# Kernel tuning notes

Hardware: AMD Instinct MI355X
Metric: run time of the kernel (lower is better)

## Reference

```python
import jax, jax.numpy as jnp
import numpy as np

BN_EPS = 1e-5


def setup_inputs() -> dict:
    key = jax.random.key(0)
    ks = jax.random.split(key, 14)
    B, N, C, NS = 2, 1024, 512, 64
    seed_xyz = jax.random.uniform(ks[0], (B, N, 3), jnp.float32)          # points in unit cube
    seed_features = jax.random.normal(ks[1], (B, C, N), jnp.float32)
    # per-seed rotation matrices (orthonormalized via QR)
    rot = jnp.linalg.qr(jax.random.normal(ks[2], (B, N, 3, 3), jnp.float32))[0]
    # cuboid extents sized so each query finds a reasonable neighbor count
    crop_size = 0.2 + 0.3 * jax.random.uniform(ks[3], (B, N, 3), jnp.float32)
    W1 = jax.random.normal(ks[4], (256, 3 + C), jnp.float32) / np.float32(np.sqrt(3 + C))
    gamma1 = 1.0 + 0.1 * jax.random.normal(ks[5], (256,), jnp.float32)
    beta1 = 0.1 * jax.random.normal(ks[6], (256,), jnp.float32)
    mean1 = 0.1 * jax.random.normal(ks[7], (256,), jnp.float32)
    var1 = 0.5 + jax.random.uniform(ks[8], (256,), jnp.float32)
    W2 = jax.random.normal(ks[9], (256, 256), jnp.float32) / np.float32(16.0)
    gamma2 = 1.0 + 0.1 * jax.random.normal(ks[10], (256,), jnp.float32)
    beta2 = 0.1 * jax.random.normal(ks[11], (256,), jnp.float32)
    mean2 = 0.1 * jax.random.normal(ks[12], (256,), jnp.float32)
    var2 = 0.5 + jax.random.uniform(ks[13], (256,), jnp.float32)
    return dict(seed_xyz=seed_xyz, seed_features=seed_features, rot=rot,
                crop_size=crop_size, W1=W1, gamma1=gamma1, beta1=beta1,
                mean1=mean1, var1=var1, W2=W2, gamma2=gamma2, beta2=beta2,
                mean2=mean2, var2=var2, nsample=NS)


def _conv_bn_relu(x, W, g, b, m, v):
    # 1x1 conv (no bias, bn=True) + inference BatchNorm + ReLU
    y = jnp.einsum('bpnc,oc->bpno', x, W)
    scale = g * jax.lax.rsqrt(v + BN_EPS)
    return jax.nn.relu((y - m) * scale + b)


def reference(seed_xyz, seed_features, rot, crop_size,
              W1, gamma1, beta1, mean1, var1,
              W2, gamma2, beta2, mean2, var2, nsample):
    # ---- rotated rectangular query + group (queries == points == seed_xyz) ----
    # diff[b,p,n] = xyz[b,n] - query[b,p]; rotate into the query's local frame
    diff = seed_xyz[:, None, :, :] - seed_xyz[:, :, None, :]          # (B,P,N,3)
    local = jnp.einsum('bpnj,bpjk->bpnk', diff, rot)                  # (B,P,N,3)
    inside = jnp.all(jnp.abs(local) <= 0.5 * crop_size[:, :, None, :], axis=-1)  # (B,P,N)
    # first `nsample` in-region indices, invalid slots filled with the first hit
    order = jnp.argsort(jnp.where(inside, 0, 1).astype(jnp.int32), axis=-1, stable=True)
    idx = order[..., :nsample]                                        # (B,P,NS)
    valid = jnp.take_along_axis(inside, idx, axis=-1)
    idx = jnp.where(valid, idx, idx[..., :1])
    # gather rotated local xyz and features
    g_xyz = jnp.take_along_axis(local, idx[..., None], axis=2)        # (B,P,NS,3)
    feats = jnp.swapaxes(seed_features, 1, 2)                         # (B,N,C)
    g_feat = jax.vmap(lambda f, i: f[i])(feats, idx)                  # (B,P,NS,C)
    grouped = jnp.concatenate([g_xyz, g_feat], axis=-1)               # (B,P,NS,3+C)
    # ---- SharedMLP (1x1 conv + BN + ReLU) x2, then max over samples ----
    h = _conv_bn_relu(grouped, W1, gamma1, beta1, mean1, var1)
    h = _conv_bn_relu(h, W2, gamma2, beta2, mean2, var2)
    out = jnp.max(h, axis=2)                                          # (B,P,256)
    return jnp.swapaxes(out, 1, 2)                                    # (B,256,P)
```

## Files before the change

### kernel.cpp

```cpp
#include <hip/hip_runtime.h>
#include <hip/hip_bf16.h>
#include <math.h>

typedef __attribute__((ext_vector_type(8))) __bf16 bf16x8;
typedef __attribute__((ext_vector_type(4))) __bf16 bf16x4;
typedef __attribute__((ext_vector_type(2))) __bf16 bf16x2;
typedef __attribute__((ext_vector_type(4))) float f32x4;

#define NPTS 1024
#define CIN 512
#define NSAMP 64
#define LDFT 520
#define LDFO 136

__device__ __forceinline__ void local_coords(const float* q, float cx, float cy, float cz,
                                             const float R[9], float& l0, float& l1, float& l2) {
    float d0 = __fsub_rn(q[0], cx);
    float d1 = __fsub_rn(q[1], cy);
    float d2 = __fsub_rn(q[2], cz);
    l0 = __fadd_rn(__fadd_rn(__fmul_rn(d0, R[0]), __fmul_rn(d1, R[3])), __fmul_rn(d2, R[6]));
    l1 = __fadd_rn(__fadd_rn(__fmul_rn(d0, R[1]), __fmul_rn(d1, R[4])), __fmul_rn(d2, R[7]));
    l2 = __fadd_rn(__fadd_rn(__fmul_rn(d0, R[2]), __fmul_rn(d1, R[5])), __fmul_rn(d2, R[8]));
}

__global__ __launch_bounds__(256) void setup_kernel(
    const float* __restrict__ xyz, const float* __restrict__ rot,
    const float* __restrict__ crop,
    const float* __restrict__ W1, const float* __restrict__ W2,
    const float* __restrict__ g1, const float* __restrict__ be1,
    const float* __restrict__ m1, const float* __restrict__ v1,
    const float* __restrict__ g2, const float* __restrict__ be2,
    const float* __restrict__ m2, const float* __restrict__ v2,
    __bf16* __restrict__ W1f, __bf16* __restrict__ W2s,
    float* __restrict__ wxs,
    float* __restrict__ s1, float* __restrict__ b1,
    float* __restrict__ s2, float* __restrict__ b2,
    unsigned short* __restrict__ seln_g) {
    __shared__ unsigned long long msk[16];
    __shared__ int wpre[17];
    __shared__ int selr[NSAMP];

    const int t = threadIdx.x;
    if (blockIdx.x < 256) {
        const int o = blockIdx.x;
        if (t == 0) {
            float sc1 = g1[o] / sqrtf(v1[o] + 1e-5f);
            s1[o] = sc1;
            b1[o] = be1[o] - m1[o] * sc1;
            float sc2 = g2[o] / sqrtf(v2[o] + 1e-5f);
            s2[o] = sc2;
            b2[o] = be2[o] - m2[o] * sc2;
            wxs[o * 4 + 0] = sc1 * W1[o * 515 + 0];
            wxs[o * 4 + 1] = sc1 * W1[o * 515 + 1];
            wxs[o * 4 + 2] = sc1 * W1[o * 515 + 2];
            wxs[o * 4 + 3] = 0.f;
        }
        for (int k = t; k < CIN; k += blockDim.x)
            W1f[o * CIN + k] = (__bf16)W1[o * 515 + 3 + k];
        {
            const int f = o * 256 + t;
            const int j = f & 7;
            const int l = (f >> 3) & 63;
            const int nt = (f >> 9) & 1;
            const int ks = (f >> 10) & 7;
            const int w = (f >> 13) & 7;
            const int o2 = w * 32 + nt * 16 + (l & 15);
            const int k = ks * 32 + ((l >> 4) << 3) + j;
            W2s[f] = (__bf16)W2[o2 * 256 + k];
        }
        return;
    }
    const int bid = blockIdx.x - 256;
    const int b = bid >> 10;
    const int l = t & 63, w = t >> 6;

    const float cx = xyz[bid * 3 + 0], cy = xyz[bid * 3 + 1], cz = xyz[bid * 3 + 2];
    float R[9];
#pragma unroll
    for (int j = 0; j < 9; ++j) R[j] = rot[bid * 9 + j];
    const float h0 = 0.5f * crop[bid * 3 + 0];
    const float h1 = 0.5f * crop[bid * 3 + 1];
    const float h2 = 0.5f * crop[bid * 3 + 2];

#pragma unroll
    for (int i = 0; i < 4; ++i) {
        const int n = i * 256 + t;
        float l0, l1, l2;
        local_coords(xyz + (size_t)(b * NPTS + n) * 3, cx, cy, cz, R, l0, l1, l2);
        bool ins = (__builtin_fabsf(l0) <= h0) && (__builtin_fabsf(l1) <= h1) &&
                   (__builtin_fabsf(l2) <= h2);
        unsigned long long bal = __ballot(ins);
        if (l == 0) msk[i * 4 + w] = bal;
    }
    __syncthreads();
    if (t < 64) {
        const int c = (t < 16) ? __popcll(msk[t]) : 0;
        int sum = c;
#pragma unroll
        for (int d = 1; d < 16; d <<= 1) {
            int v = __shfl_up(sum, d);
            if (t >= d) sum += v;
        }
        if (t < 16) wpre[t] = sum - c;
        if (t == 15) wpre[16] = sum;
    }
    __syncthreads();
    const int cnt = wpre[16];
#pragma unroll
    for (int i = 0; i < 4; ++i) {
        const int n = i * 256 + t;
        const unsigned long long wd = msk[n >> 6];
        const int bit = n & 63;
        if ((wd >> bit) & 1ull) {
            int rank = wpre[n >> 6] + __popcll(wd & ((1ull << bit) - 1ull));
            if (rank < NSAMP) selr[rank] = n;
        }
    }
    __syncthreads();
    if (t < NSAMP) {
        const int n = (t < cnt) ? selr[t] : selr[0];
        seln_g[(size_t)bid * NSAMP + t] = (unsigned short)n;
    }
}

__global__ __launch_bounds__(256) void fgemm_kernel(const float* __restrict__ feats,
                                                    const __bf16* __restrict__ W1f,
                                                    const float* __restrict__ s1,
                                                    const float* __restrict__ b1,
                                                    __bf16* __restrict__ Fsb) {
    __shared__ __align__(16) __bf16 Ft[16][LDFT];
    __shared__ __align__(16) __bf16 Fo[16][LDFO];
    const int t = threadIdx.x;
    const int b = blockIdx.x >> 7;
    const int half = (blockIdx.x >> 6) & 1;
    const int n0 = (blockIdx.x & 63) << 4;
    const int l = t & 63, w = t >> 6;
    const int lo = l & 15, kg = l >> 4;

    const float* fb = feats + (size_t)b * (CIN * NPTS) + n0;

    {
        const int n = t & 15;
        const int cq = (t >> 4) * 2;
        for (int i = 0; i < 16; ++i) {
            int c = i * 32 + cq;
            float v0 = fb[(size_t)c * NPTS + n];
            float v1 = fb[(size_t)(c + 1) * NPTS + n];
            bf16x2 pk = {(__bf16)v0, (__bf16)v1};
            *(bf16x2*)(&Ft[n][c]) = pk;
        }
    }
    __syncthreads();

    f32x4 acc[2];
#pragma unroll
    for (int mt = 0; mt < 2; ++mt) acc[mt] = f32x4{0.f, 0.f, 0.f, 0.f};

#pragma unroll
    for (int ks = 0; ks < 16; ++ks) {
        const int kk = ks * 32 + kg * 8;
        const bf16x8 bfr = *(const bf16x8*)(&Ft[lo][kk]);
#pragma unroll
        for (int mt = 0; mt < 2; ++mt) {
            const int o = half * 128 + w * 32 + mt * 16 + lo;
            const bf16x8 af = *(const bf16x8*)(&W1f[(size_t)o * CIN + kk]);
            acc[mt] = __builtin_amdgcn_mfma_f32_16x16x32_bf16(af, bfr, acc[mt], 0, 0, 0);
        }
    }
    __syncthreads();
#pragma unroll
    for (int mt = 0; mt < 2; ++mt) {
        const int ol = w * 32 + mt * 16 + kg * 4;
        const f32x4 sv = *(const f32x4*)(&s1[half * 128 + ol]);
        const f32x4 bv = *(const f32x4*)(&b1[half * 128 + ol]);
        bf16x4 r;
#pragma unroll
        for (int j = 0; j < 4; ++j) r[j] = (__bf16)fmaf(acc[mt][j], sv[j], bv[j]);
        *(bf16x4*)(&Fo[lo][ol]) = r;
    }
    __syncthreads();
    {
        const int row = t >> 4, c = t & 15;
        const bf16x8 v = *(const bf16x8*)(&Fo[row][c * 8]);
        *(bf16x8*)(&Fsb[((size_t)(b * NPTS + n0 + row)) * 256 + half * 128 + c * 8]) = v;
    }
}

__global__ __launch_bounds__(512, 2) void fused_kernel(
    const float* __restrict__ xyz, const float* __restrict__ rot,
    const __bf16* __restrict__ Fsb, const float* __restrict__ wxs,
    const unsigned short* __restrict__ seln_g,
    const __bf16* __restrict__ W2s, const float* __restrict__ s2g, const float* __restrict__ b2g,
    float* __restrict__ out) {
    __shared__ __align__(16) char A2raw[NSAMP * 512];
    __shared__ __align__(16) f32x4 lcb[NSAMP];
    __shared__ __align__(16) float outst[256][4];

    const int raw = (int)blockIdx.x;
    const int pg = (raw & 7) * 64 + (raw >> 3);
    const int b = pg >> 8;
    const int p0 = (pg & 255) * 4;
    const int t = threadIdx.x;
    const int l = t & 63, w = t >> 6;
    const int lo = l & 15, kg = l >> 4;

    bf16x8 wf[8][2];
#pragma unroll
    for (int ks = 0; ks < 8; ++ks)
#pragma unroll
        for (int nt = 0; nt < 2; ++nt)
            wf[ks][nt] = *(const bf16x8*)(&W2s[(size_t)((((w * 8 + ks) * 2 + nt) * 64) + l) * 8]);

    const int oc = (t & 31) * 8;
    const int sg = t >> 5;
    f32x4 wv[8];
#pragma unroll
    for (int j = 0; j < 8; ++j) wv[j] = *(const f32x4*)(&wxs[(oc + j) * 4]);

    float sc[2], bb[2];
#pragma unroll
    for (int nt = 0; nt < 2; ++nt) {
        const int o = w * 32 + nt * 16 + lo;
        sc[nt] = s2g[o];
        bb[nt] = b2g[o];
    }

    bf16x8 stg[4];

    {
        const int p = p0;
        if (t < NSAMP) {
            const int n = (int)seln_g[((size_t)(b * NPTS + p)) * 64 + t];
            const int bid = b * NPTS + p;
            const float cx = xyz[bid * 3 + 0], cy = xyz[bid * 3 + 1], cz = xyz[bid * 3 + 2];
            float R[9];
#pragma unroll
            for (int j = 0; j < 9; ++j) R[j] = rot[bid * 9 + j];
            float l0, l1, l2;
            local_coords(xyz + (size_t)(b * NPTS + n) * 3, cx, cy, cz, R, l0, l1, l2);
            lcb[t] = f32x4{l0, l1, l2, 0.f};
        }
#pragma unroll
        for (int si = 0; si < 4; ++si) {
            const int s = sg * 4 + si;
            const int n = (int)seln_g[((size_t)(b * NPTS + p)) * 64 + s];
            stg[si] = *(const bf16x8*)(&Fsb[((size_t)(b * NPTS + n)) * 256 + oc]);
        }
        __syncthreads();
#pragma unroll
        for (int si = 0; si < 4; ++si) {
            const int s = sg * 4 + si;
            const f32x4 cd = lcb[s];
            bf16x8 pk;
#pragma unroll
            for (int j = 0; j < 8; ++j) {
                const float x = fmaf(cd.x, wv[j].x,
                                     fmaf(cd.y, wv[j].y, fmaf(cd.z, wv[j].z, (float)stg[si][j])));
                pk[j] = (__bf16)fmaxf(x, 0.f);
            }
            *(bf16x8*)(A2raw + s * 512 + ((oc * 2) ^ ((s & 7) << 4))) = pk;
        }
        __syncthreads();
    }

    for (int pi = 0; pi < 4; ++pi) {
        if (pi < 3) {
            const int p = p0 + pi + 1;
            if (t < NSAMP) {
                const int n = (int)seln_g[((size_t)(b * NPTS + p)) * 64 + t];
                const int bid = b * NPTS + p;
                const float cx = xyz[bid * 3 + 0], cy = xyz[bid * 3 + 1], cz = xyz[bid * 3 + 2];
                float R[9];
#pragma unroll
                for (int j = 0; j < 9; ++j) R[j] = rot[bid * 9 + j];
                float l0, l1, l2;
                local_coords(xyz + (size_t)(b * NPTS + n) * 3, cx, cy, cz, R, l0, l1, l2);
                lcb[t] = f32x4{l0, l1, l2, 0.f};
            }
#pragma unroll
            for (int si = 0; si < 4; ++si) {
                const int s = sg * 4 + si;
                const int n = (int)seln_g[((size_t)(b * NPTS + p)) * 64 + s];
                stg[si] = *(const bf16x8*)(&Fsb[((size_t)(b * NPTS + n)) * 256 + oc]);
            }
        }

        f32x4 acc[4][2];
#pragma unroll
        for (int mt = 0; mt < 4; ++mt)
#pragma unroll
            for (int nt = 0; nt < 2; ++nt)
                acc[mt][nt] = f32x4{0.f, 0.f, 0.f, 0.f};

#pragma unroll
        for (int ks = 0; ks < 8; ++ks) {
            const int kkb = ks * 64 + kg * 16;
            bf16x8 af[4];
#pragma unroll
            for (int mt = 0; mt < 4; ++mt) {
                const int row = mt * 16 + lo;
                af[mt] = *(const bf16x8*)(A2raw + row * 512 + (kkb ^ ((row & 7) << 4)));
            }
#pragma unroll
            for (int nt = 0; nt < 2; ++nt)
#pragma unroll
                for (int mt = 0; mt < 4; ++mt)
                    acc[mt][nt] = __builtin_amdgcn_mfma_f32_16x16x32_bf16(af[mt], wf[ks][nt],
                                                                          acc[mt][nt], 0, 0, 0);
        }

#pragma unroll
        for (int nt = 0; nt < 2; ++nt) {
            float mx = 0.f;
#pragma unroll
            for (int mt = 0; mt < 4; ++mt)
#pragma unroll
                for (int r = 0; r < 4; ++r)
                    mx = fmaxf(mx, fmaxf(fmaf(acc[mt][nt][r], sc[nt], bb[nt]), 0.f));
            mx = fmaxf(mx, __shfl_xor(mx, 16));
            mx = fmaxf(mx, __shfl_xor(mx, 32));
            if (kg == 0) outst[w * 32 + nt * 16 + lo][pi] = mx;
        }
        __syncthreads();

        if (pi < 3) {
#pragma unroll
            for (int si = 0; si < 4; ++si) {
                const int s = sg * 4 + si;
                const f32x4 cd = lcb[s];
                bf16x8 pk;
#pragma unroll
                for (int j = 0; j < 8; ++j) {
                    const float x = fmaf(cd.x, wv[j].x,
                                         fmaf(cd.y, wv[j].y, fmaf(cd.z, wv[j].z, (float)stg[si][j])));
                    pk[j] = (__bf16)fmaxf(x, 0.f);
                }
                *(bf16x8*)(A2raw + s * 512 + ((oc * 2) ^ ((s & 7) << 4))) = pk;
            }
        }
        __syncthreads();
    }

    if (t < 256) {
        const int o = t;
        const f32x4 v = *(const f32x4*)(&outst[o][0]);
        *(f32x4*)(&out[((size_t)b * 256 + o) * NPTS + p0]) = v;
    }
}

extern "C" void kernel_launch(void* const* d_in, const int* in_sizes, int n_in,
                              void* d_out, int out_size, void* d_ws, size_t ws_size,
                              hipStream_t stream) {
    (void)in_sizes; (void)n_in; (void)out_size; (void)ws_size;
    const float* xyz   = (const float*)d_in[0];
    const float* feats = (const float*)d_in[1];
    const float* rot   = (const float*)d_in[2];
    const float* crop  = (const float*)d_in[3];
    const float* W1    = (const float*)d_in[4];
    const float* g1    = (const float*)d_in[5];
    const float* be1   = (const float*)d_in[6];
    const float* m1    = (const float*)d_in[7];
    const float* v1    = (const float*)d_in[8];
    const float* W2    = (const float*)d_in[9];
    const float* g2    = (const float*)d_in[10];
    const float* be2   = (const float*)d_in[11];
    const float* m2    = (const float*)d_in[12];
    const float* v2    = (const float*)d_in[13];

    char* ws = (char*)d_ws;
    __bf16* W1f = (__bf16*)(ws + 0);
    __bf16* W2s = (__bf16*)(ws + 262144);
    float*  wxs = (float*)(ws + 393216);
    float*  s1  = (float*)(ws + 397312);
    float*  b1  = (float*)(ws + 398336);
    float*  s2  = (float*)(ws + 399360);
    float*  b2  = (float*)(ws + 400384);
    __bf16* Fsb = (__bf16*)(ws + 401408);
    unsigned short* seln = (unsigned short*)(ws + 1449984);

    setup_kernel<<<2304, 256, 0, stream>>>(xyz, rot, crop,
                                           W1, W2, g1, be1, m1, v1, g2, be2, m2, v2,
                                           W1f, W2s, wxs, s1, b1, s2, b2, seln);
    fgemm_kernel<<<256, 256, 0, stream>>>(feats, W1f, s1, b1, Fsb);
    fused_kernel<<<512, 512, 0, stream>>>(xyz, rot, Fsb, wxs, seln, W2s, s2, b2,
                                          (float*)d_out);
}
```

Baseline: 44.05 us.

## Fuse ball-query selection into main kernel and skip empty sample tiles

Removes the separate setup kernel. The rectangular query, prefix scan and neighbor selection now run inside the fused kernel, which handles 8 query points per block instead of 4. The fused kernel also computes BN scales and converts W2 to bf16 directly from the raw inputs, and a tiny kernel converts only W1. MFMA tiles beyond the actual in-region count are skipped, which avoids redundant rows that would only duplicate the first hit. The trade-off is more per-block prologue work, redundant weight conversion in every block, and half as many blocks.

Result: slower. 51.52 us (+17.0%).

```diff
diff --git a/kernel.cpp b/kernel.cpp
--- a/kernel.cpp
+++ b/kernel.cpp
@@ -23,113 +23,27 @@
     l2 = __fadd_rn(__fadd_rn(__fmul_rn(d0, R[2]), __fmul_rn(d1, R[5])), __fmul_rn(d2, R[8]));
 }
 
-__global__ __launch_bounds__(256) void setup_kernel(
-    const float* __restrict__ xyz, const float* __restrict__ rot,
-    const float* __restrict__ crop,
-    const float* __restrict__ W1, const float* __restrict__ W2,
-    const float* __restrict__ g1, const float* __restrict__ be1,
-    const float* __restrict__ m1, const float* __restrict__ v1,
-    const float* __restrict__ g2, const float* __restrict__ be2,
-    const float* __restrict__ m2, const float* __restrict__ v2,
-    __bf16* __restrict__ W1f, __bf16* __restrict__ W2s,
-    float* __restrict__ wxs,
-    float* __restrict__ s1, float* __restrict__ b1,
-    float* __restrict__ s2, float* __restrict__ b2,
-    unsigned short* __restrict__ seln_g) {
-    __shared__ unsigned long long msk[16];
-    __shared__ int wpre[17];
-    __shared__ int selr[NSAMP];
-
-    const int t = threadIdx.x;
-    if (blockIdx.x < 256) {
-        const int o = blockIdx.x;
-        if (t == 0) {
-            float sc1 = g1[o] / sqrtf(v1[o] + 1e-5f);
-            s1[o] = sc1;
-            b1[o] = be1[o] - m1[o] * sc1;
-            float sc2 = g2[o] / sqrtf(v2[o] + 1e-5f);
-            s2[o] = sc2;
-            b2[o] = be2[o] - m2[o] * sc2;
-            wxs[o * 4 + 0] = sc1 * W1[o * 515 + 0];
-            wxs[o * 4 + 1] = sc1 * W1[o * 515 + 1];
-            wxs[o * 4 + 2] = sc1 * W1[o * 515 + 2];
-            wxs[o * 4 + 3] = 0.f;
-        }
-        for (int k = t; k < CIN; k += blockDim.x)
-            W1f[o * CIN + k] = (__bf16)W1[o * 515 + 3 + k];
-        {
-            const int f = o * 256 + t;
-            const int j = f & 7;
-            const int l = (f >> 3) & 63;
-            const int nt = (f >> 9) & 1;
-            const int ks = (f >> 10) & 7;
-            const int w = (f >> 13) & 7;
-            const int o2 = w * 32 + nt * 16 + (l & 15);
-            const int k = ks * 32 + ((l >> 4) << 3) + j;
-            W2s[f] = (__bf16)W2[o2 * 256 + k];
-        }
-        return;
-    }
-    const int bid = blockIdx.x - 256;
-    const int b = bid >> 10;
-    const int l = t & 63, w = t >> 6;
-
-    const float cx = xyz[bid * 3 + 0], cy = xyz[bid * 3 + 1], cz = xyz[bid * 3 + 2];
-    float R[9];
-#pragma unroll
-    for (int j = 0; j < 9; ++j) R[j] = rot[bid * 9 + j];
-    const float h0 = 0.5f * crop[bid * 3 + 0];
-    const float h1 = 0.5f * crop[bid * 3 + 1];
-    const float h2 = 0.5f * crop[bid * 3 + 2];
-
-#pragma unroll
-    for (int i = 0; i < 4; ++i) {
-        const int n = i * 256 + t;
-        float l0, l1, l2;
-        local_coords(xyz + (size_t)(b * NPTS + n) * 3, cx, cy, cz, R, l0, l1, l2);
-        bool ins = (__builtin_fabsf(l0) <= h0) && (__builtin_fabsf(l1) <= h1) &&
-                   (__builtin_fabsf(l2) <= h2);
-        unsigned long long bal = __ballot(ins);
-        if (l == 0) msk[i * 4 + w] = bal;
-    }
-    __syncthreads();
-    if (t < 64) {
-        const int c = (t < 16) ? __popcll(msk[t]) : 0;
-        int sum = c;
-#pragma unroll
-        for (int d = 1; d < 16; d <<= 1) {
-            int v = __shfl_up(sum, d);
-            if (t >= d) sum += v;
-        }
-        if (t < 16) wpre[t] = sum - c;
-        if (t == 15) wpre[16] = sum;
-    }
-    __syncthreads();
-    const int cnt = wpre[16];
-#pragma unroll
-    for (int i = 0; i < 4; ++i) {
-        const int n = i * 256 + t;
-        const unsigned long long wd = msk[n >> 6];
-        const int bit = n & 63;
-        if ((wd >> bit) & 1ull) {
-            int rank = wpre[n >> 6] + __popcll(wd & ((1ull << bit) - 1ull));
-            if (rank < NSAMP) selr[rank] = n;
-        }
-    }
-    __syncthreads();
-    if (t < NSAMP) {
-        const int n = (t < cnt) ? selr[t] : selr[0];
-        seln_g[(size_t)bid * NSAMP + t] = (unsigned short)n;
-    }
+__global__ __launch_bounds__(256) void w1cvt_kernel(const float* __restrict__ W1,
+                                                    __bf16* __restrict__ W1f) {
+    const int i4 = ((int)blockIdx.x * 256 + (int)threadIdx.x) * 4;
+    const int row = i4 >> 9, c = i4 & 511;
+    const float* src = W1 + (size_t)row * 515 + 3 + c;
+    bf16x4 v;
+#pragma unroll
+    for (int j = 0; j < 4; ++j) v[j] = (__bf16)src[j];
+    *(bf16x4*)(&W1f[i4]) = v;
 }
 
 __global__ __launch_bounds__(256) void fgemm_kernel(const float* __restrict__ feats,
                                                     const __bf16* __restrict__ W1f,
-                                                    const float* __restrict__ s1,
-                                                    const float* __restrict__ b1,
+                                                    const float* __restrict__ g1,
+                                                    const float* __restrict__ be1,
+                                                    const float* __restrict__ m1,
+                                                    const float* __restrict__ v1,
                                                     __bf16* __restrict__ Fsb) {
     __shared__ __align__(16) __bf16 Ft[16][LDFT];
     __shared__ __align__(16) __bf16 Fo[16][LDFO];
+    __shared__ float s1l[128], b1l[128];
     const int t = threadIdx.x;
     const int b = blockIdx.x >> 7;
     const int half = (blockIdx.x >> 6) & 1;
@@ -137,16 +51,22 @@
     const int l = t & 63, w = t >> 6;
     const int lo = l & 15, kg = l >> 4;
 
+    if (t < 128) {
+        const int o = half * 128 + t;
+        const float s = g1[o] / sqrtf(v1[o] + 1e-5f);
+        s1l[t] = s;
+        b1l[t] = be1[o] - m1[o] * s;
+    }
+
     const float* fb = feats + (size_t)b * (CIN * NPTS) + n0;
-
     {
         const int n = t & 15;
         const int cq = (t >> 4) * 2;
         for (int i = 0; i < 16; ++i) {
             int c = i * 32 + cq;
             float v0 = fb[(size_t)c * NPTS + n];
-            float v1 = fb[(size_t)(c + 1) * NPTS + n];
-            bf16x2 pk = {(__bf16)v0, (__bf16)v1};
+            float v1v = fb[(size_t)(c + 1) * NPTS + n];
+            bf16x2 pk = {(__bf16)v0, (__bf16)v1v};
             *(bf16x2*)(&Ft[n][c]) = pk;
         }
     }
@@ -171,8 +91,8 @@
 #pragma unroll
     for (int mt = 0; mt < 2; ++mt) {
         const int ol = w * 32 + mt * 16 + kg * 4;
-        const f32x4 sv = *(const f32x4*)(&s1[half * 128 + ol]);
-        const f32x4 bv = *(const f32x4*)(&b1[half * 128 + ol]);
+        const f32x4 sv = *(const f32x4*)(&s1l[ol]);
+        const f32x4 bv = *(const f32x4*)(&b1l[ol]);
         bf16x4 r;
 #pragma unroll
         for (int j = 0; j < 4; ++j) r[j] = (__bf16)fmaf(acc[mt][j], sv[j], bv[j]);
@@ -188,18 +108,25 @@
 
 __global__ __launch_bounds__(512, 2) void fused_kernel(
     const float* __restrict__ xyz, const float* __restrict__ rot,
-    const __bf16* __restrict__ Fsb, const float* __restrict__ wxs,
-    const unsigned short* __restrict__ seln_g,
-    const __bf16* __restrict__ W2s, const float* __restrict__ s2g, const float* __restrict__ b2g,
+    const float* __restrict__ crop,
+    const float* __restrict__ W1, const float* __restrict__ W2,
+    const float* __restrict__ g1, const float* __restrict__ v1,
+    const float* __restrict__ g2, const float* __restrict__ be2,
+    const float* __restrict__ m2, const float* __restrict__ v2,
+    const __bf16* __restrict__ Fsb,
     float* __restrict__ out) {
     __shared__ __align__(16) char A2raw[NSAMP * 512];
-    __shared__ __align__(16) f32x4 lcb[NSAMP];
-    __shared__ __align__(16) float outst[256][4];
+    __shared__ __align__(16) f32x4 lcsel[8][NSAMP];
+    __shared__ __align__(16) float outst[256][8];
+    __shared__ unsigned long long msk8[8][16];
+    __shared__ int wpre8[8][17];
+    __shared__ int sel8[8][NSAMP];
+    __shared__ int cnt8[8];
 
     const int raw = (int)blockIdx.x;
-    const int pg = (raw & 7) * 64 + (raw >> 3);
-    const int b = pg >> 8;
-    const int p0 = (pg & 255) * 4;
+    const int pg = (raw & 7) * 32 + (raw >> 3);
+    const int b = pg >> 7;
+    const int p0 = (pg & 127) * 8;
     const int t = threadIdx.x;
     const int l = t & 63, w = t >> 6;
     const int lo = l & 15, kg = l >> 4;
@@ -208,80 +135,145 @@
 #pragma unroll
     for (int ks = 0; ks < 8; ++ks)
 #pragma unroll
-        for (int nt = 0; nt < 2; ++nt)
-            wf[ks][nt] = *(const bf16x8*)(&W2s[(size_t)((((w * 8 + ks) * 2 + nt) * 64) + l) * 8]);
+        for (int nt = 0; nt < 2; ++nt) {
+            const int o2 = w * 32 + nt * 16 + lo;
+            const int k = ks * 32 + kg * 8;
+            const f32x4 a = *(const f32x4*)(&W2[(size_t)o2 * 256 + k]);
+            const f32x4 c = *(const f32x4*)(&W2[(size_t)o2 * 256 + k + 4]);
+            bf16x8 v;
+#pragma unroll
+            for (int j = 0; j < 4; ++j) { v[j] = (__bf16)a[j]; v[4 + j] = (__bf16)c[j]; }
+            wf[ks][nt] = v;
+        }
 
     const int oc = (t & 31) * 8;
     const int sg = t >> 5;
     f32x4 wv[8];
 #pragma unroll
-    for (int j = 0; j < 8; ++j) wv[j] = *(const f32x4*)(&wxs[(oc + j) * 4]);
+    for (int j = 0; j < 8; ++j) {
+        const int o = oc + j;
+        const float s1 = g1[o] / sqrtf(v1[o] + 1e-5f);
+        wv[j] = f32x4{s1 * W1[(size_t)o * 515 + 0], s1 * W1[(size_t)o * 515 + 1],
+                      s1 * W1[(size_t)o * 515 + 2], 0.f};
+    }
 
     float sc[2], bb[2];
 #pragma unroll
     for (int nt = 0; nt < 2; ++nt) {
         const int o = w * 32 + nt * 16 + lo;
-        sc[nt] = s2g[o];
-        bb[nt] = b2g[o];
-    }
-
-    bf16x8 stg[4];
-
-    {
-        const int p = p0;
-        if (t < NSAMP) {
-            const int n = (int)seln_g[((size_t)(b * NPTS + p)) * 64 + t];
-            const int bid = b * NPTS + p;
-            const float cx = xyz[bid * 3 + 0], cy = xyz[bid * 3 + 1], cz = xyz[bid * 3 + 2];
-            float R[9];
-#pragma unroll
-            for (int j = 0; j < 9; ++j) R[j] = rot[bid * 9 + j];
+        const float s2 = g2[o] / sqrtf(v2[o] + 1e-5f);
+        sc[nt] = s2;
+        bb[nt] = be2[o] - m2[o] * s2;
+    }
+
+    unsigned ins_bits = 0;
+#pragma unroll
+    for (int pi = 0; pi < 8; ++pi) {
+        const int bidp = b * NPTS + p0 + pi;
+        const float cx = xyz[bidp * 3 + 0], cy = xyz[bidp * 3 + 1], cz = xyz[bidp * 3 + 2];
+        float R[9];
+#pragma unroll
+        for (int j = 0; j < 9; ++j) R[j] = rot[bidp * 9 + j];
+        const float h0 = 0.5f * crop[bidp * 3 + 0];
+        const float h1 = 0.5f * crop[bidp * 3 + 1];
+        const float h2 = 0.5f * crop[bidp * 3 + 2];
+#pragma unroll
+        for (int i = 0; i < 2; ++i) {
+            const int n = i * 512 + t;
             float l0, l1, l2;
             local_coords(xyz + (size_t)(b * NPTS + n) * 3, cx, cy, cz, R, l0, l1, l2);
-            lcb[t] = f32x4{l0, l1, l2, 0.f};
-        }
+            bool ins = (__builtin_fabsf(l0) <= h0) && (__builtin_fabsf(l1) <= h1) &&
+                       (__builtin_fabsf(l2) <= h2);
+            unsigned long long bal = __ballot(ins);
+            if (l == 0) msk8[pi][i * 8 + w] = bal;
+            ins_bits |= ((unsigned)ins) << (pi * 2 + i);
+        }
+    }
+    __syncthreads();
+    {
+        const int pi = w;
+        int c = (l < 16) ? __popcll(msk8[pi][l]) : 0;
+        int sum = c;
+#pragma unroll
+        for (int d = 1; d < 16; d <<= 1) {
+            int v = __shfl_up(sum, d);
+            if (l >= d) sum += v;
+        }
+        if (l < 16) wpre8[pi][l] = sum - c;
+        if (l == 15) cnt8[pi] = sum;
+    }
+    __syncthreads();
+#pragma unroll
+    for (int pi = 0; pi < 8; ++pi) {
+#pragma unroll
+        for (int i = 0; i < 2; ++i) {
+            if ((ins_bits >> (pi * 2 + i)) & 1u) {
+                const int n = i * 512 + t;
+                const unsigned long long wd = msk8[pi][n >> 6];
+                const int rank = wpre8[pi][n >> 6] +
+                                 __popcll(wd & ((1ull << (n & 63)) - 1ull));
+                if (rank < NSAMP) {
+                    const int bidp = b * NPTS + p0 + pi;
+                    const float cx = xyz[bidp * 3 + 0], cy = xyz[bidp * 3 + 1],
+                                cz = xyz[bidp * 3 + 2];
+                    float R[9];
+#pragma unroll
+                    for (int j = 0; j < 9; ++j) R[j] = rot[bidp * 9 + j];
+                    float l0, l1, l2;
+                    local_coords(xyz + (size_t)(b * NPTS + n) * 3, cx, cy, cz, R, l0, l1, l2);
+                    sel8[pi][rank] = n;
+                    lcsel[pi][rank] = f32x4{l0, l1, l2, 0.f};
+                }
+            }
+        }
+    }
+    __syncthreads();
+
+    bf16x8 stg[4];
+    {
+        const int rn = min(cnt8[0], NSAMP);
+        const int rpad = (rn + 15) & ~15;
 #pragma unroll
         for (int si = 0; si < 4; ++si) {
             const int s = sg * 4 + si;
-            const int n = (int)seln_g[((size_t)(b * NPTS + p)) * 64 + s];
-            stg[si] = *(const bf16x8*)(&Fsb[((size_t)(b * NPTS + n)) * 256 + oc]);
-        }
-        __syncthreads();
+            if (s < rpad) {
+                const int n = (s < rn) ? sel8[0][s] : sel8[0][0];
+                stg[si] = *(const bf16x8*)(&Fsb[((size_t)(b * NPTS + n)) * 256 + oc]);
+            }
+        }
 #pragma unroll
         for (int si = 0; si < 4; ++si) {
             const int s = sg * 4 + si;
-            const f32x4 cd = lcb[s];
-            bf16x8 pk;
-#pragma unroll
-            for (int j = 0; j < 8; ++j) {
-                const float x = fmaf(cd.x, wv[j].x,
-                                     fmaf(cd.y, wv[j].y, fmaf(cd.z, wv[j].z, (float)stg[si][j])));
-                pk[j] = (__bf16)fmaxf(x, 0.f);
-            }
-            *(bf16x8*)(A2raw + s * 512 + ((oc * 2) ^ ((s & 7) << 4))) = pk;
-        }
-        __syncthreads();
-    }
-
-    for (int pi = 0; pi < 4; ++pi) {
-        if (pi < 3) {
-            const int p = p0 + pi + 1;
-            if (t < NSAMP) {
-                const int n = (int)seln_g[((size_t)(b * NPTS + p)) * 64 + t];
-                const int bid = b * NPTS + p;
-                const float cx = xyz[bid * 3 + 0], cy = xyz[bid * 3 + 1], cz = xyz[bid * 3 + 2];
-                float R[9];
-#pragma unroll
-                for (int j = 0; j < 9; ++j) R[j] = rot[bid * 9 + j];
-                float l0, l1, l2;
-                local_coords(xyz + (size_t)(b * NPTS + n) * 3, cx, cy, cz, R, l0, l1, l2);
-                lcb[t] = f32x4{l0, l1, l2, 0.f};
-            }
+            if (s < rpad) {
+                const f32x4 cd = (s < rn) ? lcsel[0][s] : lcsel[0][0];
+                bf16x8 pk;
+#pragma unroll
+                for (int j = 0; j < 8; ++j) {
+                    const float x = fmaf(cd.x, wv[j].x,
+                                         fmaf(cd.y, wv[j].y,
+                                              fmaf(cd.z, wv[j].z, (float)stg[si][j])));
+                    pk[j] = (__bf16)fmaxf(x, 0.f);
+                }
+                *(bf16x8*)(A2raw + s * 512 + ((oc * 2) ^ ((s & 7) << 4))) = pk;
+            }
+        }
+    }
+    __syncthreads();
+
+    for (int pi = 0; pi < 8; ++pi) {
+        const int mtmax = (min(cnt8[pi], NSAMP) + 15) >> 4;
+
+        int rpadn = 0, rn_next = 0;
+        if (pi < 7) {
+            rn_next = min(cnt8[pi + 1], NSAMP);
+            rpadn = (rn_next + 15) & ~15;
 #pragma unroll
             for (int si = 0; si < 4; ++si) {
                 const int s = sg * 4 + si;
-                const int n = (int)seln_g[((size_t)(b * NPTS + p)) * 64 + s];
-                stg[si] = *(const bf16x8*)(&Fsb[((size_t)(b * NPTS + n)) * 256 + oc]);
+                if (s < rpadn) {
+                    const int n = (s < rn_next) ? sel8[pi + 1][s] : sel8[pi + 1][0];
+                    stg[si] = *(const bf16x8*)(&Fsb[((size_t)(b * NPTS + n)) * 256 + oc]);
+                }
             }
         }
 
@@ -293,58 +285,63 @@
                 acc[mt][nt] = f32x4{0.f, 0.f, 0.f, 0.f};
 
 #pragma unroll
-        for (int ks = 0; ks < 8; ++ks) {
-            const int kkb = ks * 64 + kg * 16;
-            bf16x8 af[4];
-#pragma unroll
-            for (int mt = 0; mt < 4; ++mt) {
+        for (int mt = 0; mt < 4; ++mt) {
+            if (mt < mtmax) {
                 const int row = mt * 16 + lo;
-                af[mt] = *(const bf16x8*)(A2raw + row * 512 + (kkb ^ ((row & 7) << 4)));
-            }
-#pragma unroll
-            for (int nt = 0; nt < 2; ++nt)
-#pragma unroll
-                for (int mt = 0; mt < 4; ++mt)
-                    acc[mt][nt] = __builtin_amdgcn_mfma_f32_16x16x32_bf16(af[mt], wf[ks][nt],
-                                                                          acc[mt][nt], 0, 0, 0);
+#pragma unroll
+                for (int ks = 0; ks < 8; ++ks) {
+                    const bf16x8 a = *(const bf16x8*)(A2raw + row * 512 +
+                                                      ((ks * 64 + kg * 16) ^ ((row & 7) << 4)));
+                    acc[mt][0] = __builtin_amdgcn_mfma_f32_16x16x32_bf16(a, wf[ks][0],
+                                                                         acc[mt][0], 0, 0, 0);
+                    acc[mt][1] = __builtin_amdgcn_mfma_f32_16x16x32_bf16(a, wf[ks][1],
+                                                                         acc[mt][1], 0, 0, 0);
+                }
+            }
         }
 
 #pragma unroll
         for (int nt = 0; nt < 2; ++nt) {
             float mx = 0.f;
 #pragma unroll
-            for (int mt = 0; mt < 4; ++mt)
-#pragma unroll
-                for (int r = 0; r < 4; ++r)
-                    mx = fmaxf(mx, fmaxf(fmaf(acc[mt][nt][r], sc[nt], bb[nt]), 0.f));
+            for (int mt = 0; mt < 4; ++mt) {
+                if (mt < mtmax) {
+#pragma unroll
+                    for (int r = 0; r < 4; ++r)
+                        mx = fmaxf(mx, fmaxf(fmaf(acc[mt][nt][r], sc[nt], bb[nt]), 0.f));
+                }
+            }
             mx = fmaxf(mx, __shfl_xor(mx, 16));
             mx = fmaxf(mx, __shfl_xor(mx, 32));
             if (kg == 0) outst[w * 32 + nt * 16 + lo][pi] = mx;
         }
         __syncthreads();
 
-        if (pi < 3) {
+        if (pi < 7) {
 #pragma unroll
             for (int si = 0; si < 4; ++si) {
                 const int s = sg * 4 + si;
-                const f32x4 cd = lcb[s];
-                bf16x8 pk;
-#pragma unroll
-                for (int j = 0; j < 8; ++j) {
-                    const float x = fmaf(cd.x, wv[j].x,
-                                         fmaf(cd.y, wv[j].y, fmaf(cd.z, wv[j].z, (float)stg[si][j])));
-                    pk[j] = (__bf16)fmaxf(x, 0.f);
-                }
-                *(bf16x8*)(A2raw + s * 512 + ((oc * 2) ^ ((s & 7) << 4))) = pk;
+                if (s < rpadn) {
+                    const f32x4 cd = (s < rn_next) ? lcsel[pi + 1][s] : lcsel[pi + 1][0];
+                    bf16x8 pk;
+#pragma unroll
+                    for (int j = 0; j < 8; ++j) {
+                        const float x = fmaf(cd.x, wv[j].x,
+                                             fmaf(cd.y, wv[j].y,
+                                                  fmaf(cd.z, wv[j].z, (float)stg[si][j])));
+                        pk[j] = (__bf16)fmaxf(x, 0.f);
+                    }
+                    *(bf16x8*)(A2raw + s * 512 + ((oc * 2) ^ ((s & 7) << 4))) = pk;
+                }
             }
         }
         __syncthreads();
     }
 
-    if (t < 256) {
-        const int o = t;
-        const f32x4 v = *(const f32x4*)(&outst[o][0]);
-        *(f32x4*)(&out[((size_t)b * 256 + o) * NPTS + p0]) = v;
+    {
+        const int o = t >> 1, hf = t & 1;
+        const f32x4 v = *(const f32x4*)(&outst[o][hf * 4]);
+        *(f32x4*)(&out[((size_t)b * 256 + o) * NPTS + p0 + hf * 4]) = v;
     }
 }
 
@@ -369,19 +366,10 @@
 
     char* ws = (char*)d_ws;
     __bf16* W1f = (__bf16*)(ws + 0);
-    __bf16* W2s = (__bf16*)(ws + 262144);
-    float*  wxs = (float*)(ws + 393216);
-    float*  s1  = (float*)(ws + 397312);
-    float*  b1  = (float*)(ws + 398336);
-    float*  s2  = (float*)(ws + 399360);
-    float*  b2  = (float*)(ws + 400384);
-    __bf16* Fsb = (__bf16*)(ws + 401408);
-    unsigned short* seln = (unsigned short*)(ws + 1449984);
-
-    setup_kernel<<<2304, 256, 0, stream>>>(xyz, rot, crop,
-                                           W1, W2, g1, be1, m1, v1, g2, be2, m2, v2,
-                                           W1f, W2s, wxs, s1, b1, s2, b2, seln);
-    fgemm_kernel<<<256, 256, 0, stream>>>(feats, W1f, s1, b1, Fsb);
-    fused_kernel<<<512, 512, 0, stream>>>(xyz, rot, Fsb, wxs, seln, W2s, s2, b2,
-                                          (float*)d_out);
-}
+    __bf16* Fsb = (__bf16*)(ws + 262144);
+
+    w1cvt_kernel<<<128, 256, 0, stream>>>(W1, W1f);
+    fgemm_kernel<<<256, 256, 0, stream>>>(feats, W1f, g1, be1, m1, v1, Fsb);
+    fused_kernel<<<256, 512, 0, stream>>>(xyz, rot, crop, W1, W2, g1, v1, g2, be2, m2, v2,
+                                          Fsb, (float*)d_out);
+}
```

## Skip padded duplicate samples in fused MLP and precompute local coords in setup

Applied to the files above, without the earlier changes.

The setup kernel now stores each query's neighbor count and the rotated local coordinates of its selected neighbors, so the fused kernel no longer recomputes rotations from xyz/rot. The fused kernel preloads the selection indices, coordinates and counts for its four queries into shared memory. It then skips gathers, layer-1 epilogue work and second-layer MFMA tiles for rows beyond the valid count rounded up to 16. This relies on padded slots duplicating the first hit, which cannot change the max. It adds a global write and read of the coordinate buffer and branches whose benefit depends on how many neighbors each query has.

New measurement: 46.53 us. +5.6%, slower.

```diff
diff --git a/kernel.cpp b/kernel.cpp
--- a/kernel.cpp
+++ b/kernel.cpp
@@ -35,7 +35,9 @@
     float* __restrict__ wxs,
     float* __restrict__ s1, float* __restrict__ b1,
     float* __restrict__ s2, float* __restrict__ b2,
-    unsigned short* __restrict__ seln_g) {
+    unsigned short* __restrict__ seln_g, int* __restrict__ cnt_g,
+    f32x4* __restrict__ lcsel_g) {
+    __shared__ __align__(16) f32x4 lcall[NPTS];
     __shared__ unsigned long long msk[16];
     __shared__ int wpre[17];
     __shared__ int selr[NSAMP];
@@ -87,6 +89,7 @@
         const int n = i * 256 + t;
         float l0, l1, l2;
         local_coords(xyz + (size_t)(b * NPTS + n) * 3, cx, cy, cz, R, l0, l1, l2);
+        lcall[n] = f32x4{l0, l1, l2, 0.f};
         bool ins = (__builtin_fabsf(l0) <= h0) && (__builtin_fabsf(l1) <= h1) &&
                    (__builtin_fabsf(l2) <= h2);
         unsigned long long bal = __ballot(ins);
@@ -118,9 +121,11 @@
     }
     __syncthreads();
     if (t < NSAMP) {
-        const int n = (t < cnt) ? selr[t] : selr[0];
+        const int n = selr[(t < cnt) ? t : 0];
         seln_g[(size_t)bid * NSAMP + t] = (unsigned short)n;
-    }
+        lcsel_g[(size_t)bid * NSAMP + t] = lcall[n];
+    }
+    if (t == 0) cnt_g[bid] = cnt;
 }
 
 __global__ __launch_bounds__(256) void fgemm_kernel(const float* __restrict__ feats,
@@ -138,15 +143,14 @@
     const int lo = l & 15, kg = l >> 4;
 
     const float* fb = feats + (size_t)b * (CIN * NPTS) + n0;
-
     {
         const int n = t & 15;
         const int cq = (t >> 4) * 2;
         for (int i = 0; i < 16; ++i) {
             int c = i * 32 + cq;
             float v0 = fb[(size_t)c * NPTS + n];
-            float v1 = fb[(size_t)(c + 1) * NPTS + n];
-            bf16x2 pk = {(__bf16)v0, (__bf16)v1};
+            float v1v = fb[(size_t)(c + 1) * NPTS + n];
+            bf16x2 pk = {(__bf16)v0, (__bf16)v1v};
             *(bf16x2*)(&Ft[n][c]) = pk;
         }
     }
@@ -187,14 +191,16 @@
 }
 
 __global__ __launch_bounds__(512, 2) void fused_kernel(
-    const float* __restrict__ xyz, const float* __restrict__ rot,
     const __bf16* __restrict__ Fsb, const float* __restrict__ wxs,
-    const unsigned short* __restrict__ seln_g,
+    const unsigned short* __restrict__ seln_g, const int* __restrict__ cnt_g,
+    const f32x4* __restrict__ lcsel_g,
     const __bf16* __restrict__ W2s, const float* __restrict__ s2g, const float* __restrict__ b2g,
     float* __restrict__ out) {
     __shared__ __align__(16) char A2raw[NSAMP * 512];
-    __shared__ __align__(16) f32x4 lcb[NSAMP];
+    __shared__ __align__(16) f32x4 lcL[4][NSAMP];
     __shared__ __align__(16) float outst[256][4];
+    __shared__ unsigned short selL[4][NSAMP];
+    __shared__ int cntL[4];
 
     const int raw = (int)blockIdx.x;
     const int pg = (raw & 7) * 64 + (raw >> 3);
@@ -204,6 +210,14 @@
     const int l = t & 63, w = t >> 6;
     const int lo = l & 15, kg = l >> 4;
 
+    if (t < 256) {
+        const int pi = t >> 6, s = t & 63;
+        const size_t base = ((size_t)(b * NPTS + p0 + pi)) * NSAMP + s;
+        selL[pi][s] = seln_g[base];
+        lcL[pi][s] = lcsel_g[base];
+    }
+    if (t >= 256 && t < 260) cntL[t - 256] = cnt_g[b * NPTS + p0 + (t - 256)];
+
     bf16x8 wf[8][2];
 #pragma unroll
     for (int ks = 0; ks < 8; ++ks)
@@ -224,64 +238,51 @@
         sc[nt] = s2g[o];
         bb[nt] = b2g[o];
     }
+    __syncthreads();
 
     bf16x8 stg[4];
-
     {
-        const int p = p0;
-        if (t < NSAMP) {
-            const int n = (int)seln_g[((size_t)(b * NPTS + p)) * 64 + t];
-            const int bid = b * NPTS + p;
-            const float cx = xyz[bid * 3 + 0], cy = xyz[bid * 3 + 1], cz = xyz[bid * 3 + 2];
-            float R[9];
-#pragma unroll
-            for (int j = 0; j < 9; ++j) R[j] = rot[bid * 9 + j];
-            float l0, l1, l2;
-            local_coords(xyz + (size_t)(b * NPTS + n) * 3, cx, cy, cz, R, l0, l1, l2);
-            lcb[t] = f32x4{l0, l1, l2, 0.f};
-        }
+        const int rpad = (min(cntL[0], NSAMP) + 15) & ~15;
 #pragma unroll
         for (int si = 0; si < 4; ++si) {
             const int s = sg * 4 + si;
-            const int n = (int)seln_g[((size_t)(b * NPTS + p)) * 64 + s];
-            stg[si] = *(const bf16x8*)(&Fsb[((size_t)(b * NPTS + n)) * 256 + oc]);
-        }
-        __syncthreads();
+            if (s < rpad) {
+                const int n = (int)selL[0][s];
+                stg[si] = *(const bf16x8*)(&Fsb[((size_t)(b * NPTS + n)) * 256 + oc]);
+            }
+        }
 #pragma unroll
         for (int si = 0; si < 4; ++si) {
             const int s = sg * 4 + si;
-            const f32x4 cd = lcb[s];
-            bf16x8 pk;
-#pragma unroll
-            for (int j = 0; j < 8; ++j) {
-                const float x = fmaf(cd.x, wv[j].x,
-                                     fmaf(cd.y, wv[j].y, fmaf(cd.z, wv[j].z, (float)stg[si][j])));
-                pk[j] = (__bf16)fmaxf(x, 0.f);
-            }
-            *(bf16x8*)(A2raw + s * 512 + ((oc * 2) ^ ((s & 7) << 4))) = pk;
-        }
-        __syncthreads();
-    }
+            if (s < rpad) {
+                const f32x4 cd = lcL[0][s];
+                bf16x8 pk;
+#pragma unroll
+                for (int j = 0; j < 8; ++j) {
+                    const float x = fmaf(cd.x, wv[j].x,
+                                         fmaf(cd.y, wv[j].y,
+                                              fmaf(cd.z, wv[j].z, (float)stg[si][j])));
+                    pk[j] = (__bf16)fmaxf(x, 0.f);
+                }
+                *(bf16x8*)(A2raw + s * 512 + ((oc * 2) ^ ((s & 7) << 4))) = pk;
+            }
+        }
+    }
+    __syncthreads();
 
     for (int pi = 0; pi < 4; ++pi) {
+        const int mtmax = (min(cntL[pi], NSAMP) + 15) >> 4;
+
+        int rpadn = 0;
         if (pi < 3) {
-            const int p = p0 + pi + 1;
-            if (t < NSAMP) {
-                const int n = (int)seln_g[((size_t)(b * NPTS + p)) * 64 + t];
-                const int bid = b * NPTS + p;
-                const float cx = xyz[bid * 3 + 0], cy = xyz[bid * 3 + 1], cz = xyz[bid * 3 + 2];
-                float R[9];
-#pragma unroll
-                for (int j = 0; j < 9; ++j) R[j] = rot[bid * 9 + j];
-                float l0, l1, l2;
-                local_coords(xyz + (size_t)(b * NPTS + n) * 3, cx, cy, cz, R, l0, l1, l2);
-                lcb[t] = f32x4{l0, l1, l2, 0.f};
-            }
+            rpadn = (min(cntL[pi + 1], NSAMP) + 15) & ~15;
 #pragma unroll
             for (int si = 0; si < 4; ++si) {
                 const int s = sg * 4 + si;
-                const int n = (int)seln_g[((size_t)(b * NPTS + p)) * 64 + s];
-                stg[si] = *(const bf16x8*)(&Fsb[((size_t)(b * NPTS + n)) * 256 + oc]);
+                if (s < rpadn) {
+                    const int n = (int)selL[pi + 1][s];
+                    stg[si] = *(const bf16x8*)(&Fsb[((size_t)(b * NPTS + n)) * 256 + oc]);
+                }
             }
         }
 
@@ -293,30 +294,32 @@
                 acc[mt][nt] = f32x4{0.f, 0.f, 0.f, 0.f};
 
 #pragma unroll
-        for (int ks = 0; ks < 8; ++ks) {
-            const int kkb = ks * 64 + kg * 16;
-            bf16x8 af[4];
-#pragma unroll
-            for (int mt = 0; mt < 4; ++mt) {
+        for (int mt = 0; mt < 4; ++mt) {
+            if (mt < mtmax) {
                 const int row = mt * 16 + lo;
-                af[mt] = *(const bf16x8*)(A2raw + row * 512 + (kkb ^ ((row & 7) << 4)));
-            }
-#pragma unroll
-            for (int nt = 0; nt < 2; ++nt)
-#pragma unroll
-                for (int mt = 0; mt < 4; ++mt)
-                    acc[mt][nt] = __builtin_amdgcn_mfma_f32_16x16x32_bf16(af[mt], wf[ks][nt],
-                                                                          acc[mt][nt], 0, 0, 0);
+#pragma unroll
+                for (int ks = 0; ks < 8; ++ks) {
+                    const bf16x8 a = *(const bf16x8*)(A2raw + row * 512 +
+                                                      ((ks * 64 + kg * 16) ^ ((row & 7) << 4)));
+                    acc[mt][0] = __builtin_amdgcn_mfma_f32_16x16x32_bf16(a, wf[ks][0],
+                                                                         acc[mt][0], 0, 0, 0);
+                    acc[mt][1] = __builtin_amdgcn_mfma_f32_16x16x32_bf16(a, wf[ks][1],
+                                                                         acc[mt][1], 0, 0, 0);
+                }
+            }
         }
 
 #pragma unroll
         for (int nt = 0; nt < 2; ++nt) {
             float mx = 0.f;
 #pragma unroll
-            for (int mt = 0; mt < 4; ++mt)
-#pragma unroll
-                for (int r = 0; r < 4; ++r)
-                    mx = fmaxf(mx, fmaxf(fmaf(acc[mt][nt][r], sc[nt], bb[nt]), 0.f));
+            for (int mt = 0; mt < 4; ++mt) {
+                if (mt < mtmax) {
+#pragma unroll
+                    for (int r = 0; r < 4; ++r)
+                        mx = fmaxf(mx, fmaxf(fmaf(acc[mt][nt][r], sc[nt], bb[nt]), 0.f));
+                }
+            }
             mx = fmaxf(mx, __shfl_xor(mx, 16));
             mx = fmaxf(mx, __shfl_xor(mx, 32));
             if (kg == 0) outst[w * 32 + nt * 16 + lo][pi] = mx;
@@ -327,15 +330,18 @@
 #pragma unroll
             for (int si = 0; si < 4; ++si) {
                 const int s = sg * 4 + si;
-                const f32x4 cd = lcb[s];
-                bf16x8 pk;
-#pragma unroll
-                for (int j = 0; j < 8; ++j) {
-                    const float x = fmaf(cd.x, wv[j].x,
-                                         fmaf(cd.y, wv[j].y, fmaf(cd.z, wv[j].z, (float)stg[si][j])));
-                    pk[j] = (__bf16)fmaxf(x, 0.f);
-                }
-                *(bf16x8*)(A2raw + s * 512 + ((oc * 2) ^ ((s & 7) << 4))) = pk;
+                if (s < rpadn) {
+                    const f32x4 cd = lcL[pi + 1][s];
+                    bf16x8 pk;
+#pragma unroll
+                    for (int j = 0; j < 8; ++j) {
+                        const float x = fmaf(cd.x, wv[j].x,
+                                             fmaf(cd.y, wv[j].y,
+                                                  fmaf(cd.z, wv[j].z, (float)stg[si][j])));
+                        pk[j] = (__bf16)fmaxf(x, 0.f);
+                    }
+                    *(bf16x8*)(A2raw + s * 512 + ((oc * 2) ^ ((s & 7) << 4))) = pk;
+                }
             }
         }
         __syncthreads();
@@ -377,11 +383,13 @@
     float*  b2  = (float*)(ws + 400384);
     __bf16* Fsb = (__bf16*)(ws + 401408);
     unsigned short* seln = (unsigned short*)(ws + 1449984);
+    int*    cntg = (int*)(ws + 1712128);
+    f32x4*  lcse = (f32x4*)(ws + 1720320);
 
     setup_kernel<<<2304, 256, 0, stream>>>(xyz, rot, crop,
                                            W1, W2, g1, be1, m1, v1, g2, be2, m2, v2,
-                                           W1f, W2s, wxs, s1, b1, s2, b2, seln);
+                                           W1f, W2s, wxs, s1, b1, s2, b2, seln, cntg, lcse);
     fgemm_kernel<<<256, 256, 0, stream>>>(feats, W1f, s1, b1, Fsb);
-    fused_kernel<<<512, 512, 0, stream>>>(xyz, rot, Fsb, wxs, seln, W2s, s2, b2,
+    fused_kernel<<<512, 512, 0, stream>>>(Fsb, wxs, seln, cntg, lcse, W2s, s2, b2,
                                           (float*)d_out);
 }
```
